# Performance work log

Hardware: AMD Instinct MI355X
Metric: run time of the kernel (lower is better)

The kernel has to match this reference:

```python
import jax, jax.numpy as jnp
import numpy as np

B, S, IN, H, L = 64, 512, 512, 1024, 2


def setup_inputs() -> dict:
    key = jax.random.key(0)
    ks = jax.random.split(key, 3 + 6 * L)
    inp = {
        "seq": jax.random.normal(ks[0], (B, S, IN), jnp.float32),
        "d_seq": jax.random.normal(ks[1], (B, S, 1), jnp.float32),
        "lq_seq": jax.random.normal(ks[2], (B, S, 1), jnp.float32),
    }
    for l in range(L):
        in_l = IN if l == 0 else H
        k = ks[3 + 6 * l: 3 + 6 * (l + 1)]
        sc_mod = 1.0 / np.sqrt(H + 2)
        sc_cell = 1.0 / np.sqrt(H)
        inp[f"modW{l}"] = jax.random.uniform(k[0], (in_l, H + 2), jnp.float32, -sc_mod, sc_mod)
        inp[f"modb{l}"] = jax.random.uniform(k[1], (in_l,), jnp.float32, -sc_mod, sc_mod)
        inp[f"Wih{l}"] = jax.random.uniform(k[2], (4 * H, in_l), jnp.float32, -sc_cell, sc_cell)
        inp[f"Whh{l}"] = jax.random.uniform(k[3], (4 * H, H), jnp.float32, -sc_cell, sc_cell)
        inp[f"bih{l}"] = jax.random.uniform(k[4], (4 * H,), jnp.float32, -sc_cell, sc_cell)
        inp[f"bhh{l}"] = jax.random.uniform(k[5], (4 * H,), jnp.float32, -sc_cell, sc_cell)
    return inp


def _cell_layer(seq, d_seq, lq_seq, modW, modb, Wih, Whh, bih, bhh):
    # seq: [B,S,in], d_seq/lq_seq: [B,S,1]
    b = seq.shape[0]
    h0 = jnp.zeros((b, H), seq.dtype)
    c0 = jnp.zeros((b, H), seq.dtype)

    def step(carry, xt):
        h, c = carry
        x, dt, lqt = xt  # [B,in], [B,1], [B,1]
        gate_in = jnp.concatenate([h, dt, lqt], axis=1)  # [B, H+2]
        m = jax.nn.sigmoid(gate_in @ modW.T + modb)      # [B, in]
        gates = (m * x) @ Wih.T + bih + h @ Whh.T + bhh  # [B, 4H]
        i, f, g, o = jnp.split(gates, 4, axis=1)
        c = jax.nn.sigmoid(f) * c + jax.nn.sigmoid(i) * jnp.tanh(g)
        h = jax.nn.sigmoid(o) * jnp.tanh(c)
        return (h, c), h

    xs = (jnp.swapaxes(seq, 0, 1), jnp.swapaxes(d_seq, 0, 1), jnp.swapaxes(lq_seq, 0, 1))
    (h, _c), outs = jax.lax.scan(step, (h0, c0), xs)
    return jnp.swapaxes(outs, 0, 1), h  # [B,S,H], [B,H]


def reference(seq, d_seq, lq_seq,
              modW0, modb0, Wih0, Whh0, bih0, bhh0,
              modW1, modb1, Wih1, Whh1, bih1, bhh1):
    params = [(modW0, modb0, Wih0, Whh0, bih0, bhh0),
              (modW1, modb1, Wih1, Whh1, bih1, bhh1)]
    last_h = None
    for p in params:
        seq, last_h = _cell_layer(seq, d_seq, lq_seq, *p)
    return seq, last_h
```

## Files before the change

kernel.cpp:

```cpp
#include <hip/hip_runtime.h>


typedef __attribute__((ext_vector_type(8))) short short8;
typedef __attribute__((ext_vector_type(4))) float f32x4;

constexpr int B_ = 64, S_ = 512, IN_ = 512, H_ = 1024;
constexpr int NBLK = 256, NTHR = 512;
constexpr int BH = B_ * H_;
constexpr int WP = 1032;
constexpr int D_ = 4;

__device__ __forceinline__ unsigned short f2bf(float f) {
  unsigned u = __builtin_bit_cast(unsigned, f);
  u += 0x7FFFu + ((u >> 16) & 1u);
  return (unsigned short)(u >> 16);
}
__device__ __forceinline__ float bf2f(unsigned short h) {
  unsigned u = ((unsigned)h) << 16;
  return __builtin_bit_cast(float, u);
}
__device__ __forceinline__ float sigm(float x) { return 1.f / (1.f + __expf(-x)); }
__device__ __forceinline__ float tanh_(float x) {
  float e = __expf(2.f * x);
  return 1.f - 2.f / (e + 1.f);
}

__device__ __forceinline__ void store_short_wt(unsigned short* p, unsigned short v) {
  unsigned w = v;
  asm volatile("global_store_short %0, %1, off sc0 sc1" :: "v"(p), "v"(w) : "memory");
}
__device__ __forceinline__ void store_float_wt(float* p, float v) {
  asm volatile("global_store_dword %0, %1, off sc0 sc1" :: "v"(p), "v"(v) : "memory");
}
__device__ __forceinline__ int aload(int* p) {
  return __hip_atomic_load(p, __ATOMIC_RELAXED, __HIP_MEMORY_SCOPE_AGENT);
}
__device__ __forceinline__ void astore(int* p, int v) {
  __hip_atomic_store(p, v, __ATOMIC_RELAXED, __HIP_MEMORY_SCOPE_AGENT);
}

__device__ __forceinline__ void xcd_inv(int* slot, int epoch, bool islead) {
  if (islead) {
    asm volatile("buffer_inv sc1\n\ts_waitcnt vmcnt(0)" ::: "memory");
    astore(slot, epoch);
  } else {
    while (aload(slot) < epoch) {}
    asm volatile("buffer_inv sc0\n\ts_waitcnt vmcnt(0)" ::: "memory");
  }
}

__global__ __launch_bounds__(NTHR, 1) void qmog_kernel(
    const float* __restrict__ seq, const float* __restrict__ dseq,
    const float* __restrict__ lqseq,
    const float* __restrict__ modW0, const float* __restrict__ modb0,
    const float* __restrict__ Wih0, const float* __restrict__ Whh0,
    const float* __restrict__ bih0, const float* __restrict__ bhh0,
    const float* __restrict__ modW1, const float* __restrict__ modb1,
    const float* __restrict__ Wih1, const float* __restrict__ Whh1,
    const float* __restrict__ bih1, const float* __restrict__ bhh1,
    float* __restrict__ dout, int* __restrict__ flags,
    unsigned short* __restrict__ h0r, unsigned short* __restrict__ h1r,
    unsigned short* __restrict__ u0, unsigned short* __restrict__ u1) {
  __shared__ unsigned short Wih_s[32 * WP];
  __shared__ unsigned short Whh_s[32 * WP];
  __shared__ unsigned short modW_s[8 * WP];
  __shared__ float red_s[4][8][64];
  __shared__ float bias_s[32];
  __shared__ float wd_s[8], wl_s[8], mb_s[8];
  __shared__ int lead_s, xg_s;

  const int bid = blockIdx.x, tid = threadIdx.x;
  const int layer = bid >> 7;
  const int slice = bid & 127;
  const bool mblk = (slice == 0);
  const int wave = tid >> 6, lane = tid & 63;
  const int mt = wave & 3;
  const int kh = wave >> 2;
  const int Kin = layer ? H_ : IN_;
  const int KU = Kin / 32;
  const int MCB = layer ? 8 : 4;
  const int hc0 = slice * 8;
  const int mc0 = slice * MCB;
  const float* modW = layer ? modW1 : modW0;
  const float* modb = layer ? modb1 : modb0;
  const float* Wih  = layer ? Wih1 : Wih0;
  const float* Whh  = layer ? Whh1 : Whh0;
  const float* bih  = layer ? bih1 : bih0;
  const float* bhh  = layer ? bhh1 : bhh0;
  unsigned short* ubuf = layer ? u1 : u0;

  int* arrL = flags + layer * 512;
  int* goL  = arrL + 128;
  int* goL0 = flags + 128;
  int* goL1 = flags + 512 + 128;

  if (tid == 0) {
    unsigned xcc;
    asm volatile("s_getreg_b32 %0, hwreg(HW_REG_XCC_ID)" : "=s"(xcc));
    int g = layer * 8 + (int)(xcc & 7);
    xg_s = g;
    int tkt = __hip_atomic_fetch_add(&flags[1536 + g], 1, __ATOMIC_RELAXED,
                                     __HIP_MEMORY_SCOPE_AGENT);
    lead_s = (tkt == 0);
  }

  for (int idx = tid; idx < 32 * Kin; idx += NTHR) {
    int row = idx / Kin, k = idx - row * Kin;
    int grow = (row >> 3) * H_ + hc0 + (row & 7);
    Wih_s[row * WP + k] = f2bf(Wih[grow * Kin + k]);
  }
  for (int idx = tid; idx < 32 * H_; idx += NTHR) {
    int row = idx >> 10, k = idx & (H_ - 1);
    int grow = (row >> 3) * H_ + hc0 + (row & 7);
    Whh_s[row * WP + k] = f2bf(Whh[grow * H_ + k]);
  }
  for (int idx = tid; idx < MCB * H_; idx += NTHR) {
    int row = idx >> 10, k = idx & (H_ - 1);
    modW_s[row * WP + k] = f2bf(modW[(mc0 + row) * (H_ + 2) + k]);
  }
  if (tid < 32) {
    int grow = (tid >> 3) * H_ + hc0 + (tid & 7);
    bias_s[tid] = bih[grow] + bhh[grow];
  }
  if (tid < MCB) {
    wd_s[tid] = modW[(mc0 + tid) * (H_ + 2) + H_];
    wl_s[tid] = modW[(mc0 + tid) * (H_ + 2) + H_ + 1];
    mb_s[tid] = modb[mc0 + tid];
  }
  __syncthreads();
  const bool islead = (lead_s != 0);
  int* invA = &flags[1024 + xg_s * 16];
  int* invB = &flags[1280 + xg_s * 16];

  float creg0 = 0.f, creg1 = 0.f;
  const int c = lane & 15, kg = lane >> 4;
  const int cm = c & (MCB - 1);
  const bool epi = (!kh && c < MCB);
  const int ku2 = KU >> 1;

  float dtv[4], lqv[4], xvv[4];
  if (epi) {
#pragma unroll
    for (int r = 0; r < 4; ++r) {
      int b_ = mt * 16 + kg * 4 + r;
      dtv[r] = dseq[b_ * S_];
      lqv[r] = lqseq[b_ * S_];
      if (!layer) xvv[r] = seq[(b_ * S_) * IN_ + mc0 + c];
    }
  }

  for (int st = 0; st < S_; ++st) {
    if (st > 0) {
      const int epw = 2 * st;
      if (mblk) {
        if (tid < 64) {
          bool ok;
          do {
            ok = (aload(&arrL[tid]) >= epw) & (aload(&arrL[tid + 64]) >= epw);
          } while (!__all(ok));
          if (tid < 8) astore(&goL[tid << 5], epw);
        }
      } else if (tid == 0) {
        while (aload(&goL[(slice & 7) << 5]) < epw) {}
      }
    }
    if (tid == 0) {
      if (layer) {
        while (aload(&goL0[(slice & 7) << 5]) < 2 * st + 2) {}
      }
      xcd_inv(invA, st + 1, islead);
    }
    __syncthreads();

    const bool havh = (st > 0);
    short8 hv[16];
    if (havh) {
      const unsigned short* hrow =
          (layer ? h1r + ((st - 1) & 1) * BH : h0r + ((st - 1) % D_) * BH) +
          (mt * 16 + c) * H_ + kh * 512;
#pragma unroll
      for (int kk = 0; kk < 16; ++kk)
        hv[kk] = *(const short8*)(hrow + kk * 32 + kg * 8);
    }
    if (layer && epi) {
#pragma unroll
      for (int r = 0; r < 4; ++r) {
        int b_ = mt * 16 + kg * 4 + r;
        xvv[r] = bf2f(h0r[(st % D_) * BH + b_ * H_ + mc0 + c]);
      }
    }

    f32x4 mA = {0,0,0,0}, mB = {0,0,0,0};
    if (havh) {
      const unsigned short* wm = modW_s + cm * WP + kh * 512;
#pragma unroll
      for (int kk = 0; kk < 16; ++kk) {
        short8 bm = *(const short8*)(wm + kk * 32 + kg * 8);
        if (kk & 1)
          mB = __builtin_amdgcn_mfma_f32_16x16x32_bf16(hv[kk], bm, mB, 0, 0, 0);
        else
          mA = __builtin_amdgcn_mfma_f32_16x16x32_bf16(hv[kk], bm, mA, 0, 0, 0);
      }
    }
    if (kh) {
#pragma unroll
      for (int r = 0; r < 4; ++r) red_s[mt][r][lane] = mA[r] + mB[r];
    }
    __syncthreads();
    if (epi) {
      const float wd = wd_s[cm], wl = wl_s[cm], mb = mb_s[cm];
#pragma unroll
      for (int r = 0; r < 4; ++r) {
        int b_ = mt * 16 + kg * 4 + r;
        float mval = sigm(mA[r] + mB[r] + red_s[mt][r][lane] +
                          dtv[r] * wd + lqv[r] * wl + mb);
        store_short_wt(&ubuf[b_ * Kin + mc0 + c], f2bf(mval * xvv[r]));
      }
    }

    asm volatile("s_waitcnt vmcnt(0)" ::: "memory");
    __syncthreads();
    if (tid == 0) astore(&arrL[slice], 2 * st + 1);

    f32x4 p0 = {0,0,0,0}, p1 = {0,0,0,0};
    if (havh) {
      const unsigned short* w0b = Whh_s + c * WP + kh * 512;
      const unsigned short* w1b = Whh_s + (16 + c) * WP + kh * 512;
#pragma unroll
      for (int kk = 0; kk < 16; ++kk) {
        short8 w0 = *(const short8*)(w0b + kk * 32 + kg * 8);
        short8 w1 = *(const short8*)(w1b + kk * 32 + kg * 8);
        p0 = __builtin_amdgcn_mfma_f32_16x16x32_bf16(hv[kk], w0, p0, 0, 0, 0);
        p1 = __builtin_amdgcn_mfma_f32_16x16x32_bf16(hv[kk], w1, p1, 0, 0, 0);
      }
    }

    {
      const int epw = 2 * st + 1;
      if (mblk) {
        if (tid < 64) {
          bool ok;
          do {
            ok = (aload(&arrL[tid]) >= epw) & (aload(&arrL[tid + 64]) >= epw);
          } while (!__all(ok));
          if (tid < 8) astore(&goL[tid << 5], epw);
        }
      } else if (tid == 0) {
        while (aload(&goL[(slice & 7) << 5]) < epw) {}
      }
      if (tid == 0) {
        if (!layer && st >= D_) {
          while (aload(&goL1[(slice & 7) << 5]) < 2 * (st - D_) + 1) {}
        }
        xcd_inv(invB, st + 1, islead);
      }
      __syncthreads();
    }

    {
      const unsigned short* urow = ubuf + (mt * 16 + c) * Kin + kh * (ku2 * 32);
      short8 uv[16];
#pragma unroll
      for (int kk = 0; kk < 16; ++kk)
        if (kk < ku2) uv[kk] = *(const short8*)(urow + kk * 32 + kg * 8);
      f32x4 g0 = {0,0,0,0}, g1 = {0,0,0,0};
      const unsigned short* v0b = Wih_s + c * WP + kh * (ku2 * 32);
      const unsigned short* v1b = Wih_s + (16 + c) * WP + kh * (ku2 * 32);
#pragma unroll
      for (int kk = 0; kk < 16; ++kk) {
        if (kk < ku2) {
          short8 v0 = *(const short8*)(v0b + kk * 32 + kg * 8);
          short8 v1 = *(const short8*)(v1b + kk * 32 + kg * 8);
          g0 = __builtin_amdgcn_mfma_f32_16x16x32_bf16(uv[kk], v0, g0, 0, 0, 0);
          g1 = __builtin_amdgcn_mfma_f32_16x16x32_bf16(uv[kk], v1, g1, 0, 0, 0);
        }
      }
      if (kh) {
#pragma unroll
        for (int r = 0; r < 4; ++r) {
          red_s[mt][r][lane] = g0[r] + p0[r];
          red_s[mt][4 + r][lane] = g1[r] + p1[r];
        }
      }
      __syncthreads();
      if (!kh) {
        const float bia0 = bias_s[c], bia1 = bias_s[16 + c];
        f32x4 s0, s1;
#pragma unroll
        for (int r = 0; r < 4; ++r) {
          g0[r] += p0[r] + red_s[mt][r][lane] + bia0;
          g1[r] += p1[r] + red_s[mt][4 + r][lane] + bia1;
        }
#pragma unroll
        for (int r = 0; r < 4; ++r) {
          s0[r] = __shfl_xor(g0[r], 8);
          s1[r] = __shfl_xor(g1[r], 8);
        }
        const bool low = c < 8;
        const int hc = hc0 + (c & 7);
        const int rbase = low ? 0 : 2;
        unsigned short* hw = layer ? h1r + (st & 1) * BH : h0r + (st % D_) * BH;
#pragma unroll
        for (int j = 0; j < 2; ++j) {
          const int rr = rbase + j;
          float iv = low ? g0[rr] : s0[rr];
          float fv = low ? s0[rr] : g0[rr];
          float gv = low ? g1[rr] : s1[rr];
          float ov = low ? s1[rr] : g1[rr];
          float cold = j ? creg1 : creg0;
          float cn = sigm(fv) * cold + sigm(iv) * tanh_(gv);
          float hn = sigm(ov) * tanh_(cn);
          if (j) creg1 = cn; else creg0 = cn;
          int b_ = mt * 16 + kg * 4 + rr;
          store_short_wt(&hw[b_ * H_ + hc], f2bf(hn));
          if (layer) {
            store_float_wt(&dout[(b_ * S_ + st) * H_ + hc], hn);
            if (st == S_ - 1) store_float_wt(&dout[B_ * S_ * H_ + b_ * H_ + hc], hn);
          }
        }
      }
    }

    asm volatile("s_waitcnt vmcnt(0)" ::: "memory");
    __syncthreads();
    if (tid == 0) astore(&arrL[slice], 2 * st + 2);

    const int t2 = st + 1;
    if (t2 < S_ && epi) {
#pragma unroll
      for (int r = 0; r < 4; ++r) {
        int b_ = mt * 16 + kg * 4 + r;
        dtv[r] = dseq[b_ * S_ + t2];
        lqv[r] = lqseq[b_ * S_ + t2];
        if (!layer) xvv[r] = seq[(b_ * S_ + t2) * IN_ + mc0 + c];
      }
    }
  }

  if (mblk && tid < 64) {
    const int epw = 2 * S_;
    bool ok;
    do {
      ok = (aload(&arrL[tid]) >= epw) & (aload(&arrL[tid + 64]) >= epw);
    } while (!__all(ok));
    if (tid < 8) astore(&goL[tid << 5], epw);
  }
}

extern "C" void kernel_launch(void* const* d_in, const int* in_sizes, int n_in,
                              void* d_out, int out_size, void* d_ws,
                              size_t ws_size, hipStream_t stream) {
  char* w = (char*)d_ws;
  int* flags = (int*)w;
  unsigned short* h0r = (unsigned short*)(w + 16384);
  unsigned short* h1r = (unsigned short*)(w + 16384 + 524288);
  unsigned short* u0 = (unsigned short*)(w + 16384 + 524288 + 262144);
  unsigned short* u1 = (unsigned short*)(w + 16384 + 524288 + 262144 + 65536);

  hipMemsetAsync(flags, 0, 16384, stream);

  qmog_kernel<<<NBLK, NTHR, 0, stream>>>(
      (const float*)d_in[0], (const float*)d_in[1], (const float*)d_in[2],
      (const float*)d_in[3], (const float*)d_in[4], (const float*)d_in[5],
      (const float*)d_in[6], (const float*)d_in[7], (const float*)d_in[8],
      (const float*)d_in[9], (const float*)d_in[10], (const float*)d_in[11],
      (const float*)d_in[12], (const float*)d_in[13], (const float*)d_in[14],
      (float*)d_out, flags, h0r, h1r, u0, u1);
}
```

Measured before the change: 7.625 ms.

## Replace master-block flag barrier with atomic counter barrier and per-XCD leader waits

Replaces the grid barrier, in which block 0 polled 128 per-block arrival flags and broadcast go flags, with a per-layer atomic fetch-add counter. The last block to arrive publishes an all-arrived epoch. Only the per-XCD leader block waits on that epoch, then invalidates cache and signals the other blocks on its XCD. This removes the serial master hop and the per-block polling of go flags. The cost is contention on a single atomic counter per phase.

```diff
diff --git a/kernel.cpp b/kernel.cpp
--- a/kernel.cpp
+++ b/kernel.cpp
@@ -38,15 +38,8 @@
 __device__ __forceinline__ void astore(int* p, int v) {
   __hip_atomic_store(p, v, __ATOMIC_RELAXED, __HIP_MEMORY_SCOPE_AGENT);
 }
-
-__device__ __forceinline__ void xcd_inv(int* slot, int epoch, bool islead) {
-  if (islead) {
-    asm volatile("buffer_inv sc1\n\ts_waitcnt vmcnt(0)" ::: "memory");
-    astore(slot, epoch);
-  } else {
-    while (aload(slot) < epoch) {}
-    asm volatile("buffer_inv sc0\n\ts_waitcnt vmcnt(0)" ::: "memory");
-  }
+__device__ __forceinline__ int aadd(int* p) {
+  return __hip_atomic_fetch_add(p, 1, __ATOMIC_RELAXED, __HIP_MEMORY_SCOPE_AGENT);
 }
 
 __global__ __launch_bounds__(NTHR, 1) void qmog_kernel(
@@ -72,7 +65,6 @@
   const int bid = blockIdx.x, tid = threadIdx.x;
   const int layer = bid >> 7;
   const int slice = bid & 127;
-  const bool mblk = (slice == 0);
   const int wave = tid >> 6, lane = tid & 63;
   const int mt = wave & 3;
   const int kh = wave >> 2;
@@ -89,10 +81,12 @@
   const float* bhh  = layer ? bhh1 : bhh0;
   unsigned short* ubuf = layer ? u1 : u0;
 
-  int* arrL = flags + layer * 512;
-  int* goL  = arrL + 128;
-  int* goL0 = flags + 128;
-  int* goL1 = flags + 512 + 128;
+  int* allA = &flags[896 + layer * 16];
+  int* allB = &flags[928 + layer * 16];
+  int* ctrA = &flags[960 + layer * 16];
+  int* ctrB = &flags[992 + layer * 16];
+  int* allB_L0 = &flags[928];
+  int* allA_L1 = &flags[896 + 16];
 
   if (tid == 0) {
     unsigned xcc;
@@ -150,25 +144,18 @@
   }
 
   for (int st = 0; st < S_; ++st) {
-    if (st > 0) {
-      const int epw = 2 * st;
-      if (mblk) {
-        if (tid < 64) {
-          bool ok;
-          do {
-            ok = (aload(&arrL[tid]) >= epw) & (aload(&arrL[tid + 64]) >= epw);
-          } while (!__all(ok));
-          if (tid < 8) astore(&goL[tid << 5], epw);
-        }
-      } else if (tid == 0) {
-        while (aload(&goL[(slice & 7) << 5]) < epw) {}
-      }
-    }
+    const int e = st + 1;
+
     if (tid == 0) {
-      if (layer) {
-        while (aload(&goL0[(slice & 7) << 5]) < 2 * st + 2) {}
-      }
-      xcd_inv(invA, st + 1, islead);
+      if (islead) {
+        if (st > 0) while (aload(allB) < st) {}
+        if (layer) while (aload(allB_L0) < e) {}
+        asm volatile("buffer_inv sc1\n\ts_waitcnt vmcnt(0)" ::: "memory");
+        astore(invA, e);
+      } else {
+        while (aload(invA) < e) {}
+        asm volatile("buffer_inv sc0\n\ts_waitcnt vmcnt(0)" ::: "memory");
+      }
     }
     __syncthreads();
 
@@ -220,7 +207,10 @@
 
     asm volatile("s_waitcnt vmcnt(0)" ::: "memory");
     __syncthreads();
-    if (tid == 0) astore(&arrL[slice], 2 * st + 1);
+    if (tid == 0) {
+      int old = aadd(ctrA);
+      if (old == 128 * e - 1) astore(allA, e);
+    }
 
     f32x4 p0 = {0,0,0,0}, p1 = {0,0,0,0};
     if (havh) {
@@ -235,27 +225,20 @@
       }
     }
 
-    {
-      const int epw = 2 * st + 1;
-      if (mblk) {
-        if (tid < 64) {
-          bool ok;
-          do {
-            ok = (aload(&arrL[tid]) >= epw) & (aload(&arrL[tid + 64]) >= epw);
-          } while (!__all(ok));
-          if (tid < 8) astore(&goL[tid << 5], epw);
-        }
-      } else if (tid == 0) {
-        while (aload(&goL[(slice & 7) << 5]) < epw) {}
-      }
-      if (tid == 0) {
+    if (tid == 0) {
+      if (islead) {
+        while (aload(allA) < e) {}
         if (!layer && st >= D_) {
-          while (aload(&goL1[(slice & 7) << 5]) < 2 * (st - D_) + 1) {}
-        }
-        xcd_inv(invB, st + 1, islead);
-      }
-      __syncthreads();
-    }
+          while (aload(allA_L1) < st - D_ + 1) {}
+        }
+        asm volatile("buffer_inv sc1\n\ts_waitcnt vmcnt(0)" ::: "memory");
+        astore(invB, e);
+      } else {
+        while (aload(invB) < e) {}
+        asm volatile("buffer_inv sc0\n\ts_waitcnt vmcnt(0)" ::: "memory");
+      }
+    }
+    __syncthreads();
 
     {
       const unsigned short* urow = ubuf + (mt * 16 + c) * Kin + kh * (ku2 * 32);
@@ -323,7 +306,10 @@
 
     asm volatile("s_waitcnt vmcnt(0)" ::: "memory");
     __syncthreads();
-    if (tid == 0) astore(&arrL[slice], 2 * st + 2);
+    if (tid == 0) {
+      int old = aadd(ctrB);
+      if (old == 128 * e - 1) astore(allB, e);
+    }
 
     const int t2 = st + 1;
     if (t2 < S_ && epi) {
@@ -335,15 +321,6 @@
         if (!layer) xvv[r] = seq[(b_ * S_ + t2) * IN_ + mc0 + c];
       }
     }
-  }
-
-  if (mblk && tid < 64) {
-    const int epw = 2 * S_;
-    bool ok;
-    do {
-      ok = (aload(&arrL[tid]) >= epw) & (aload(&arrL[tid + 64]) >= epw);
-    } while (!__all(ok));
-    if (tid < 8) astore(&goL[tid << 5], epw);
   }
 }
 
```

After: 7.864 ms. 3.1% more time.
